# Kernel optimization log

Measured on AMD Instinct MI355X. Metric: run time of the kernel, lower is better.

The kernel has to match this reference:

```python
import jax, jax.numpy as jnp
import numpy as np

IN_DIM = 1024
OUT_DIM = 1024
SPLINE_ORDER = 3
NUM_KNOTS = 16
BATCH = 2048


def _bspline_bases(t, knots, order):
    # t: (N,) flattened inputs; knots: (NUM_KNOTS,)
    # degree-0 indicator bases, then Cox-de Boor recursion (matches torch slicing)
    tb = t[:, None]  # (N, 1) broadcasts against knot slices
    b = ((knots[:-1] <= tb) & (knots[1:] > tb)).astype(t.dtype)  # (N, NUM_KNOTS-1)
    for k in range(1, order):
        left = (tb - knots[:-k - 1]) / (knots[k:-1] - knots[:-k - 1]) * b[:, :-1]
        right = (knots[k + 1:] - tb) / (knots[k + 1:] - knots[1:-k]) * b[:, 1:]
        b = left + right
    return b  # (N, NUM_KNOTS - order)


def setup_inputs() -> dict:
    key = jax.random.key(0)
    k1, k2 = jax.random.split(key)
    x = jax.random.uniform(k1, (BATCH, IN_DIM), dtype=jnp.float32)
    spline_parameters = jax.random.normal(
        k2, (OUT_DIM, IN_DIM, NUM_KNOTS - SPLINE_ORDER), dtype=jnp.float32
    )
    w_b = jnp.array(1.0, dtype=jnp.float32)
    w_s = jnp.array(1.0, dtype=jnp.float32)
    return {"x": x, "spline_parameters": spline_parameters, "w_b": w_b, "w_s": w_s}


def reference(x, spline_parameters, w_b, w_s):
    knots = jnp.linspace(-1.0 - 2.0 / NUM_KNOTS, 1.0 + 2.0 / NUM_KNOTS, NUM_KNOTS,
                         dtype=x.dtype)
    bases = _bspline_bases(x.reshape(-1), knots, SPLINE_ORDER)  # (B*I, K)
    bases = bases.reshape(*x.shape, -1)  # (B, I, K)
    # sum over in_dim and knots directly (avoids the (B, O, I, K) intermediate);
    # equals sum_i of (w_b*silu(x)[b,i] + w_s*splines[b,o,i]) from the torch code.
    splines = jnp.einsum("bik,oik->bo", bases, spline_parameters)  # (B, O)
    silu_sum = jnp.sum(jax.nn.silu(x), axis=-1, keepdims=True)  # (B, 1)
    return w_b * silu_sum + w_s * splines
```

## Files before the change

### kernel.cpp

```cpp
#include <hip/hip_runtime.h>
#include <hip/hip_bf16.h>
#include <cstdint>
#include <cstddef>

#define IN_DIM 1024
#define OUT_DIM 1024
#define BATCH 2048
#define NSEG 8
#define K2 (IN_DIM * NSEG)

typedef float f32x4 __attribute__((ext_vector_type(4)));
typedef __bf16 bf16x8 __attribute__((ext_vector_type(8)));

__device__ __forceinline__ unsigned int f2bf(float f) {
  unsigned int u = __float_as_uint(f);
  u += 0x7FFF + ((u >> 16) & 1);
  return u >> 16;
}

__device__ __forceinline__ void gload16(const void* g, void* l) {
  __builtin_amdgcn_global_load_lds((__attribute__((address_space(1))) void*)g,
                                   (__attribute__((address_space(3))) void*)l,
                                   16, 0, 0);
}

__device__ __forceinline__ uint4 basis8(float v) {
  float u = (v + 1.125f) * (1.0f / 0.15f);
  int j = (int)floorf(u);
  j = j < 7 ? 7 : (j > 14 ? 14 : j);
  float s = u - (float)j;
  unsigned long long w0 = f2bf(0.5f * (1.f - s) * (1.f - s));
  unsigned long long w1 = f2bf(0.5f + s * (1.f - s));
  unsigned long long w2 = f2bf(0.5f * s * s);
  unsigned __int128 pack = (unsigned __int128)(w0 | (w1 << 16) | (w2 << 32))
                           << (16 * (j - 7));
  unsigned long long lo = (unsigned long long)pack;
  unsigned long long hi = (unsigned long long)(pack >> 64);
  uint4 o;
  o.x = (unsigned int)lo; o.y = (unsigned int)(lo >> 32);
  o.z = (unsigned int)hi; o.w = (unsigned int)(hi >> 32);
  return o;
}

__global__ __launch_bounds__(256) void silu_init(const float* __restrict__ x,
                                                 float* __restrict__ out,
                                                 const float* __restrict__ wbp) {
  __shared__ float red[4];
  const int b = blockIdx.x;
  const int t = threadIdx.x;
  float4 xv = ((const float4*)(x + (size_t)b * IN_DIM))[t];
  float lsum = xv.x / (1.f + __expf(-xv.x)) + xv.y / (1.f + __expf(-xv.y)) +
               xv.z / (1.f + __expf(-xv.z)) + xv.w / (1.f + __expf(-xv.w));
#pragma unroll
  for (int off = 32; off >= 1; off >>= 1) lsum += __shfl_down(lsum, off);
  if ((t & 63) == 0) red[t >> 6] = lsum;
  __syncthreads();
  float v = wbp[0] * (red[0] + red[1] + red[2] + red[3]);
  float4 vv = {v, v, v, v};
  ((float4*)(out + (size_t)b * OUT_DIM))[t] = vv;
}

__global__ __launch_bounds__(256) void prep_b(const float* __restrict__ p,
                                              short* __restrict__ B,
                                              const float* __restrict__ wsp) {
  __shared__ float ld[3328];
  const int blk = blockIdx.x;
  const int t = threadIdx.x;
  const uint4* src = (const uint4*)(p + (size_t)blk * 3328);
  uint4* l4 = (uint4*)ld;
#pragma unroll
  for (int c = 0; c < 3; ++c) l4[c * 256 + t] = src[c * 256 + t];
  if (t < 64) l4[768 + t] = src[768 + t];
  __syncthreads();
  const float* my = ld + t * 13 + 5;
  const float w = wsp[0];
  uint4 o;
  o.x = f2bf(w * my[0]) | (f2bf(w * my[1]) << 16);
  o.y = f2bf(w * my[2]) | (f2bf(w * my[3]) << 16);
  o.z = f2bf(w * my[4]) | (f2bf(w * my[5]) << 16);
  o.w = f2bf(w * my[6]) | (f2bf(w * my[7]) << 16);
  ((uint4*)B)[(size_t)blk * 256 + t] = o;
}

#define BM 64
#define BN 256
#define BK 32
#define KSPLIT 4
#define KPB (K2 / KSPLIT)
#define KSTEPS (KPB / BK)

__global__ __launch_bounds__(256) void gemm_fused(const float* __restrict__ x,
                                                  const short* __restrict__ B,
                                                  float* __restrict__ out) {
  __shared__ __bf16 As[2][BM][BK];
  __shared__ __bf16 Bs[2][BN][BK];

  const int tid = threadIdx.x;
  const int wid = tid >> 6;
  const int lane = tid & 63;
  const int bm = blockIdx.x >> 2;
  const int bn = blockIdx.x & 3;
  const int ks = blockIdx.y;
  const int row0 = bm * BM;
  const int col0 = bn * BN;
  const int kstart = ks * KPB;
  const int istart = kstart / NSEG;

  const int sr = lane >> 2;
  const int sc = (lane & 3) * 8;
  const short* bg = B + (size_t)(col0 + 64 * wid + sr) * K2 + kstart + sc;

  const float* xp = x + (size_t)(row0 + (tid >> 2)) * IN_DIM + istart + (tid & 3);

  f32x4 acc[4][4];
#pragma unroll
  for (int m = 0; m < 4; ++m)
#pragma unroll
    for (int n = 0; n < 4; ++n) acc[m][n] = (f32x4){0.f, 0.f, 0.f, 0.f};

  const int wc = 64 * wid;
  const int fr = lane & 15;
  const int fk = (lane >> 4) * 8;

#define STAGE_B(kt_, buf_)                                                    \
  {                                                                           \
    const int kb_ = (kt_)*BK;                                                 \
    _Pragma("unroll") for (int c = 0; c < 4; ++c)                             \
        gload16(bg + (size_t)(c * 16) * K2 + kb_,                             \
                &Bs[buf_][64 * wid + c * 16][0]);                             \
  }

#define COMPUTE(buf_)                                                         \
  {                                                                           \
    bf16x8 af[4], bb[4];                                                      \
    _Pragma("unroll") for (int m = 0; m < 4; ++m)                             \
        af[m] = *(const bf16x8*)&As[buf_][m * 16 + fr][fk];                   \
    _Pragma("unroll") for (int n = 0; n < 4; ++n)                             \
        bb[n] = *(const bf16x8*)&Bs[buf_][wc + n * 16 + fr][fk];              \
    _Pragma("unroll") for (int m = 0; m < 4; ++m)                             \
        _Pragma("unroll") for (int n = 0; n < 4; ++n)                         \
            acc[m][n] = __builtin_amdgcn_mfma_f32_16x16x32_bf16(              \
                af[m], bb[n], acc[m][n], 0, 0, 0);                            \
  }

#define LDS_BARRIER                                                           \
  asm volatile("s_waitcnt lgkmcnt(0)" ::: "memory");                          \
  __builtin_amdgcn_s_barrier();

  float xa = xp[0];
  float xb = xp[4];
  STAGE_B(0, 0);
  ((uint4*)As[0])[tid] = basis8(xa);
  LDS_BARRIER;

#pragma unroll 1
  for (int i = 0; i < (KSTEPS - 2) / 2; ++i) {
    const int t0 = 2 * i;
    STAGE_B(t0 + 1, 1);
    ((uint4*)As[1])[tid] = basis8(xb);
    xa = xp[(t0 + 2) * 4];
    asm volatile("s_waitcnt vmcnt(5)" ::: "memory");
    COMPUTE(0);
    LDS_BARRIER;
    STAGE_B(t0 + 2, 0);
    ((uint4*)As[0])[tid] = basis8(xa);
    xb = xp[(t0 + 3) * 4];
    asm volatile("s_waitcnt vmcnt(5)" ::: "memory");
    COMPUTE(1);
    LDS_BARRIER;
  }

  STAGE_B(KSTEPS - 1, 1);
  ((uint4*)As[1])[tid] = basis8(xb);
  asm volatile("s_waitcnt vmcnt(4)" ::: "memory");
  COMPUTE(0);
  LDS_BARRIER;

  asm volatile("s_waitcnt vmcnt(0)" ::: "memory");
  COMPUTE(1);

#undef STAGE_B
#undef COMPUTE
#undef LDS_BARRIER

  const int orow = (lane >> 4) * 4;
#pragma unroll
  for (int m = 0; m < 4; ++m)
#pragma unroll
    for (int n = 0; n < 4; ++n) {
      const int rg = row0 + m * 16 + orow;
      const int cg = col0 + wc + n * 16 + fr;
      float* op = out + (size_t)rg * OUT_DIM + cg;
#pragma unroll
      for (int r = 0; r < 4; ++r)
        atomicAdd(op + (size_t)r * OUT_DIM, acc[m][n][r]);
    }
}

extern "C" void kernel_launch(void* const* d_in, const int* in_sizes, int n_in,
                              void* d_out, int out_size, void* d_ws, size_t ws_size,
                              hipStream_t stream) {
  const float* x = (const float*)d_in[0];
  const float* p = (const float*)d_in[1];
  const float* wb = (const float*)d_in[2];
  const float* wsc = (const float*)d_in[3];
  float* out = (float*)d_out;

  short* B = (short*)d_ws;

  silu_init<<<BATCH, 256, 0, stream>>>(x, out, wb);
  prep_b<<<OUT_DIM * IN_DIM / 256, 256, 0, stream>>>(p, B, wsc);
  dim3 grid(128, KSPLIT);
  gemm_fused<<<grid, 256, 0, stream>>>(x, B, out);
}
```

Baseline: 172.3 us.

## Merge prep kernels, enlarge GEMM tile to 128x256 with triple-buffered B

Merges the SiLU init and weight-conversion kernels into one launch, which removes one kernel launch. The GEMM tile grows to BM=128 with 512 threads (8 waves in a 2x4 layout) and the K-split rises to 8. B staging moves to a triple-buffered pipeline with deeper prefetch of x values, and the block index is remapped so K-split blocks are grouped. The basis computation uses packed bf16 conversion and select-based placement in place of a 128-bit shift. This adds more atomic traffic from the higher K-split and more register pressure.

```diff
diff --git a/kernel.cpp b/kernel.cpp
--- a/kernel.cpp
+++ b/kernel.cpp
@@ -9,11 +9,18 @@
 #define NSEG 8
 #define K2 (IN_DIM * NSEG)
 
+#define BM 128
+#define BN 256
+#define BK 32
+#define KSPLIT 8
+#define KPB (K2 / KSPLIT)
+#define KSTEPS (KPB / BK)
+
 typedef float f32x4 __attribute__((ext_vector_type(4)));
 typedef __bf16 bf16x8 __attribute__((ext_vector_type(8)));
 
-__device__ __forceinline__ unsigned int f2bf(float f) {
-  unsigned int u = __float_as_uint(f);
+__device__ __forceinline__ unsigned f2bf(float f) {
+  unsigned u = __float_as_uint(f);
   u += 0x7FFF + ((u >> 16) & 1);
   return u >> 16;
 }
@@ -25,90 +32,88 @@
 }
 
 __device__ __forceinline__ uint4 basis8(float v) {
-  float u = (v + 1.125f) * (1.0f / 0.15f);
-  int j = (int)floorf(u);
-  j = j < 7 ? 7 : (j > 14 ? 14 : j);
-  float s = u - (float)j;
-  unsigned long long w0 = f2bf(0.5f * (1.f - s) * (1.f - s));
-  unsigned long long w1 = f2bf(0.5f + s * (1.f - s));
-  unsigned long long w2 = f2bf(0.5f * s * s);
-  unsigned __int128 pack = (unsigned __int128)(w0 | (w1 << 16) | (w2 << 32))
-                           << (16 * (j - 7));
-  unsigned long long lo = (unsigned long long)pack;
-  unsigned long long hi = (unsigned long long)(pack >> 64);
+  float u = __builtin_fmaf(v, 1.0f / 0.15f, 7.5f);
+  float jf = floorf(u);
+  int j = (int)jf;
+  float s = u - jf;
+  float t1 = 1.f - s;
+  float w0 = 0.5f * t1 * t1;
+  float w1 = __builtin_fmaf(s, t1, 0.5f);
+  float w2 = 0.5f * s * s;
+  unsigned d0, d1;
+  asm("v_cvt_pk_bf16_f32 %0, %1, %2" : "=v"(d0) : "v"(w0), "v"(w1));
+  asm("v_cvt_pk_bf16_f32 %0, %1, %2" : "=v"(d1) : "v"(w2), "v"(0.f));
+  int p = j - 7;
+  unsigned long long full = (((unsigned long long)d1 << 32) | d0) << ((p & 1) << 4);
+  unsigned lo = (unsigned)full, hi = (unsigned)(full >> 32);
+  int q = p >> 1;
   uint4 o;
-  o.x = (unsigned int)lo; o.y = (unsigned int)(lo >> 32);
-  o.z = (unsigned int)hi; o.w = (unsigned int)(hi >> 32);
+  o.x = q == 0 ? lo : 0u;
+  o.y = q == 1 ? lo : (q == 0 ? hi : 0u);
+  o.z = q == 2 ? lo : (q == 1 ? hi : 0u);
+  o.w = q == 3 ? lo : (q == 2 ? hi : 0u);
   return o;
 }
 
-__global__ __launch_bounds__(256) void silu_init(const float* __restrict__ x,
-                                                 float* __restrict__ out,
-                                                 const float* __restrict__ wbp) {
-  __shared__ float red[4];
-  const int b = blockIdx.x;
-  const int t = threadIdx.x;
-  float4 xv = ((const float4*)(x + (size_t)b * IN_DIM))[t];
-  float lsum = xv.x / (1.f + __expf(-xv.x)) + xv.y / (1.f + __expf(-xv.y)) +
-               xv.z / (1.f + __expf(-xv.z)) + xv.w / (1.f + __expf(-xv.w));
-#pragma unroll
-  for (int off = 32; off >= 1; off >>= 1) lsum += __shfl_down(lsum, off);
-  if ((t & 63) == 0) red[t >> 6] = lsum;
-  __syncthreads();
-  float v = wbp[0] * (red[0] + red[1] + red[2] + red[3]);
-  float4 vv = {v, v, v, v};
-  ((float4*)(out + (size_t)b * OUT_DIM))[t] = vv;
-}
-
-__global__ __launch_bounds__(256) void prep_b(const float* __restrict__ p,
-                                              short* __restrict__ B,
-                                              const float* __restrict__ wsp) {
+__global__ __launch_bounds__(256) void prep(const float* __restrict__ p,
+                                            const float* __restrict__ x,
+                                            short* __restrict__ B,
+                                            float* __restrict__ out,
+                                            const float* __restrict__ wbp,
+                                            const float* __restrict__ wsp) {
   __shared__ float ld[3328];
   const int blk = blockIdx.x;
   const int t = threadIdx.x;
-  const uint4* src = (const uint4*)(p + (size_t)blk * 3328);
-  uint4* l4 = (uint4*)ld;
-#pragma unroll
-  for (int c = 0; c < 3; ++c) l4[c * 256 + t] = src[c * 256 + t];
-  if (t < 64) l4[768 + t] = src[768 + t];
-  __syncthreads();
-  const float* my = ld + t * 13 + 5;
-  const float w = wsp[0];
-  uint4 o;
-  o.x = f2bf(w * my[0]) | (f2bf(w * my[1]) << 16);
-  o.y = f2bf(w * my[2]) | (f2bf(w * my[3]) << 16);
-  o.z = f2bf(w * my[4]) | (f2bf(w * my[5]) << 16);
-  o.w = f2bf(w * my[6]) | (f2bf(w * my[7]) << 16);
-  ((uint4*)B)[(size_t)blk * 256 + t] = o;
-}
-
-#define BM 64
-#define BN 256
-#define BK 32
-#define KSPLIT 4
-#define KPB (K2 / KSPLIT)
-#define KSTEPS (KPB / BK)
-
-__global__ __launch_bounds__(256) void gemm_fused(const float* __restrict__ x,
+  if (blk < 4096) {
+    const uint4* src = (const uint4*)(p + (size_t)blk * 3328);
+    uint4* l4 = (uint4*)ld;
+#pragma unroll
+    for (int c = 0; c < 3; ++c) l4[c * 256 + t] = src[c * 256 + t];
+    if (t < 64) l4[768 + t] = src[768 + t];
+    __syncthreads();
+    const float* my = ld + t * 13 + 5;
+    const float w = wsp[0];
+    uint4 o;
+    o.x = f2bf(w * my[0]) | (f2bf(w * my[1]) << 16);
+    o.y = f2bf(w * my[2]) | (f2bf(w * my[3]) << 16);
+    o.z = f2bf(w * my[4]) | (f2bf(w * my[5]) << 16);
+    o.w = f2bf(w * my[6]) | (f2bf(w * my[7]) << 16);
+    ((uint4*)B)[(size_t)blk * 256 + t] = o;
+  } else {
+    const int b = blk - 4096;
+    float4 xv = ((const float4*)(x + (size_t)b * IN_DIM))[t];
+    float lsum = xv.x / (1.f + __expf(-xv.x)) + xv.y / (1.f + __expf(-xv.y)) +
+                 xv.z / (1.f + __expf(-xv.z)) + xv.w / (1.f + __expf(-xv.w));
+#pragma unroll
+    for (int off = 32; off >= 1; off >>= 1) lsum += __shfl_down(lsum, off);
+    if ((t & 63) == 0) ld[t >> 6] = lsum;
+    __syncthreads();
+    float v = wbp[0] * (ld[0] + ld[1] + ld[2] + ld[3]);
+    float4 vv = {v, v, v, v};
+    ((float4*)(out + (size_t)b * OUT_DIM))[t] = vv;
+  }
+}
+
+__global__ __launch_bounds__(512) void gemm_fused(const float* __restrict__ x,
                                                   const short* __restrict__ B,
                                                   float* __restrict__ out) {
   __shared__ __bf16 As[2][BM][BK];
-  __shared__ __bf16 Bs[2][BN][BK];
+  __shared__ __bf16 Bs[3][BN][BK];
 
   const int tid = threadIdx.x;
   const int wid = tid >> 6;
   const int lane = tid & 63;
-  const int bm = blockIdx.x >> 2;
-  const int bn = blockIdx.x & 3;
-  const int ks = blockIdx.y;
+  const int bid = blockIdx.x;
+  const int ks = bid & 7;
+  const int bm = (bid >> 3) & 15;
+  const int bn = bid >> 7;
   const int row0 = bm * BM;
   const int col0 = bn * BN;
   const int kstart = ks * KPB;
   const int istart = kstart / NSEG;
 
-  const int sr = lane >> 2;
-  const int sc = (lane & 3) * 8;
-  const short* bg = B + (size_t)(col0 + 64 * wid + sr) * K2 + kstart + sc;
+  const short* bg = B + (size_t)(col0 + 32 * wid + (lane >> 2)) * K2 + kstart +
+                    (lane & 3) * 8;
 
   const float* xp = x + (size_t)(row0 + (tid >> 2)) * IN_DIM + istart + (tid & 3);
 
@@ -118,67 +123,69 @@
 #pragma unroll
     for (int n = 0; n < 4; ++n) acc[m][n] = (f32x4){0.f, 0.f, 0.f, 0.f};
 
-  const int wc = 64 * wid;
+  const int wr = (wid >> 2) * 64;
+  const int wc = (wid & 3) * 64;
   const int fr = lane & 15;
   const int fk = (lane >> 4) * 8;
 
 #define STAGE_B(kt_, buf_)                                                    \
   {                                                                           \
     const int kb_ = (kt_)*BK;                                                 \
-    _Pragma("unroll") for (int c = 0; c < 4; ++c)                             \
-        gload16(bg + (size_t)(c * 16) * K2 + kb_,                             \
-                &Bs[buf_][64 * wid + c * 16][0]);                             \
-  }
-
-#define COMPUTE(buf_)                                                         \
+    gload16(bg + kb_, &Bs[buf_][32 * wid][0]);                                \
+    gload16(bg + (size_t)16 * K2 + kb_, &Bs[buf_][32 * wid + 16][0]);         \
+  }
+
+#define COMPUTE(A_, B_)                                                       \
   {                                                                           \
-    bf16x8 af[4], bb[4];                                                      \
-    _Pragma("unroll") for (int m = 0; m < 4; ++m)                             \
-        af[m] = *(const bf16x8*)&As[buf_][m * 16 + fr][fk];                   \
-    _Pragma("unroll") for (int n = 0; n < 4; ++n)                             \
-        bb[n] = *(const bf16x8*)&Bs[buf_][wc + n * 16 + fr][fk];              \
-    _Pragma("unroll") for (int m = 0; m < 4; ++m)                             \
-        _Pragma("unroll") for (int n = 0; n < 4; ++n)                         \
-            acc[m][n] = __builtin_amdgcn_mfma_f32_16x16x32_bf16(              \
-                af[m], bb[n], acc[m][n], 0, 0, 0);                            \
+    bf16x8 af_[4], bb_[4];                                                    \
+    _Pragma("unroll") for (int m_ = 0; m_ < 4; ++m_)                          \
+        af_[m_] = *(const bf16x8*)&(A_)[wr + m_ * 16 + fr][fk];               \
+    _Pragma("unroll") for (int n_ = 0; n_ < 4; ++n_)                          \
+        bb_[n_] = *(const bf16x8*)&(B_)[wc + n_ * 16 + fr][fk];               \
+    _Pragma("unroll") for (int m_ = 0; m_ < 4; ++m_)                          \
+        _Pragma("unroll") for (int n_ = 0; n_ < 4; ++n_)                      \
+            acc[m_][n_] = __builtin_amdgcn_mfma_f32_16x16x32_bf16(            \
+                af_[m_], bb_[n_], acc[m_][n_], 0, 0, 0);                      \
   }
 
 #define LDS_BARRIER                                                           \
   asm volatile("s_waitcnt lgkmcnt(0)" ::: "memory");                          \
   __builtin_amdgcn_s_barrier();
 
-  float xa = xp[0];
-  float xb = xp[4];
+  float xc = xp[0];
   STAGE_B(0, 0);
-  ((uint4*)As[0])[tid] = basis8(xa);
+  STAGE_B(1, 1);
+  float xn0 = xp[4];
+  float xn1 = xp[8];
+  ((uint4*)As[0])[tid] = basis8(xc);
+  asm volatile("s_waitcnt vmcnt(0)" ::: "memory");
   LDS_BARRIER;
 
+  float xnew;
+#define STEP(s_)                                                              \
+  {                                                                           \
+    const int t_ = 6 * i + (s_);                                              \
+    STAGE_B(t_ + 2, ((s_) + 2) % 3);                                          \
+    ((uint4*)As[((s_) + 1) & 1])[tid] = basis8(xn0);                          \
+    { int tn_ = t_ + 3; tn_ = tn_ > 31 ? 31 : tn_; xnew = xp[tn_ * 4]; }      \
+    COMPUTE(As[(s_) & 1], Bs[(s_) % 3]);                                      \
+    asm volatile("s_waitcnt vmcnt(3)" ::: "memory");                          \
+    LDS_BARRIER;                                                              \
+    xn0 = xn1; xn1 = xnew;                                                    \
+  }
+
 #pragma unroll 1
-  for (int i = 0; i < (KSTEPS - 2) / 2; ++i) {
-    const int t0 = 2 * i;
-    STAGE_B(t0 + 1, 1);
-    ((uint4*)As[1])[tid] = basis8(xb);
-    xa = xp[(t0 + 2) * 4];
-    asm volatile("s_waitcnt vmcnt(5)" ::: "memory");
-    COMPUTE(0);
-    LDS_BARRIER;
-    STAGE_B(t0 + 2, 0);
-    ((uint4*)As[0])[tid] = basis8(xa);
-    xb = xp[(t0 + 3) * 4];
-    asm volatile("s_waitcnt vmcnt(5)" ::: "memory");
-    COMPUTE(1);
-    LDS_BARRIER;
-  }
-
-  STAGE_B(KSTEPS - 1, 1);
-  ((uint4*)As[1])[tid] = basis8(xb);
-  asm volatile("s_waitcnt vmcnt(4)" ::: "memory");
-  COMPUTE(0);
+  for (int i = 0; i < 5; ++i) {
+    STEP(0) STEP(1) STEP(2) STEP(3) STEP(4) STEP(5)
+  }
+
+  ((uint4*)As[1])[tid] = basis8(xn0);
+  COMPUTE(As[0], Bs[0]);
+  asm volatile("s_waitcnt vmcnt(0)" ::: "memory");
   LDS_BARRIER;
-
-  asm volatile("s_waitcnt vmcnt(0)" ::: "memory");
-  COMPUTE(1);
-
+  COMPUTE(As[1], Bs[1]);
+
+#undef STEP
 #undef STAGE_B
 #undef COMPUTE
 #undef LDS_BARRIER
@@ -188,7 +195,7 @@
   for (int m = 0; m < 4; ++m)
 #pragma unroll
     for (int n = 0; n < 4; ++n) {
-      const int rg = row0 + m * 16 + orow;
+      const int rg = row0 + wr + m * 16 + orow;
       const int cg = col0 + wc + n * 16 + fr;
       float* op = out + (size_t)rg * OUT_DIM + cg;
 #pragma unroll
@@ -208,8 +215,6 @@
 
   short* B = (short*)d_ws;
 
-  silu_init<<<BATCH, 256, 0, stream>>>(x, out, wb);
-  prep_b<<<OUT_DIM * IN_DIM / 256, 256, 0, stream>>>(p, B, wsc);
-  dim3 grid(128, KSPLIT);
-  gemm_fused<<<grid, 256, 0, stream>>>(x, B, out);
-}
+  prep<<<6144, 256, 0, stream>>>(p, x, B, out, wb, wsc);
+  gemm_fused<<<512, 512, 0, stream>>>(x, B, out);
+}
```

New measurement: 208.9 us. 1.21x slower.

## Merge prep kernels, double K-split, reorder block mapping, cheapen basis packing

Applied to the files above, without the earlier changes.

Merges the silu row-sum initialisation and the spline-weight bf16 conversion into one launch, with branches selected by block index. Doubles the K-split of the fused GEMM from 4 to 8 (1024 blocks) and remaps block IDs so consecutive blocks share the same output tile across K slices. The basis computation now uses packed bf16 conversion instructions and select-based placement instead of 128-bit shifts. It also adds sched_barrier fences after LDS barriers. The extra K-split doubles the atomicAdd traffic on the output in exchange for more parallelism.

```diff
diff --git a/kernel.cpp b/kernel.cpp
--- a/kernel.cpp
+++ b/kernel.cpp
@@ -9,11 +9,18 @@
 #define NSEG 8
 #define K2 (IN_DIM * NSEG)
 
+#define BM 64
+#define BN 256
+#define BK 32
+#define KSPLIT 8
+#define KPB (K2 / KSPLIT)
+#define KSTEPS (KPB / BK)
+
 typedef float f32x4 __attribute__((ext_vector_type(4)));
 typedef __bf16 bf16x8 __attribute__((ext_vector_type(8)));
 
-__device__ __forceinline__ unsigned int f2bf(float f) {
-  unsigned int u = __float_as_uint(f);
+__device__ __forceinline__ unsigned f2bf(float f) {
+  unsigned u = __float_as_uint(f);
   u += 0x7FFF + ((u >> 16) & 1);
   return u >> 16;
 }
@@ -25,69 +32,67 @@
 }
 
 __device__ __forceinline__ uint4 basis8(float v) {
-  float u = (v + 1.125f) * (1.0f / 0.15f);
-  int j = (int)floorf(u);
-  j = j < 7 ? 7 : (j > 14 ? 14 : j);
-  float s = u - (float)j;
-  unsigned long long w0 = f2bf(0.5f * (1.f - s) * (1.f - s));
-  unsigned long long w1 = f2bf(0.5f + s * (1.f - s));
-  unsigned long long w2 = f2bf(0.5f * s * s);
-  unsigned __int128 pack = (unsigned __int128)(w0 | (w1 << 16) | (w2 << 32))
-                           << (16 * (j - 7));
-  unsigned long long lo = (unsigned long long)pack;
-  unsigned long long hi = (unsigned long long)(pack >> 64);
+  float u = __builtin_fmaf(v, 1.0f / 0.15f, 7.5f);
+  float jf = floorf(u);
+  int j = (int)jf;
+  float s = u - jf;
+  float t1 = 1.f - s;
+  float w0 = 0.5f * t1 * t1;
+  float w1 = __builtin_fmaf(s, t1, 0.5f);
+  float w2 = 0.5f * s * s;
+  unsigned d0, d1;
+  asm("v_cvt_pk_bf16_f32 %0, %1, %2" : "=v"(d0) : "v"(w0), "v"(w1));
+  asm("v_cvt_pk_bf16_f32 %0, %1, %2" : "=v"(d1) : "v"(w2), "v"(0.f));
+  int p = j - 7;
+  unsigned long long full = (((unsigned long long)d1 << 32) | d0) << ((p & 1) << 4);
+  unsigned lo = (unsigned)full, hi = (unsigned)(full >> 32);
+  int q = p >> 1;
   uint4 o;
-  o.x = (unsigned int)lo; o.y = (unsigned int)(lo >> 32);
-  o.z = (unsigned int)hi; o.w = (unsigned int)(hi >> 32);
+  o.x = q == 0 ? lo : 0u;
+  o.y = q == 1 ? lo : (q == 0 ? hi : 0u);
+  o.z = q == 2 ? lo : (q == 1 ? hi : 0u);
+  o.w = q == 3 ? lo : (q == 2 ? hi : 0u);
   return o;
 }
 
-__global__ __launch_bounds__(256) void silu_init(const float* __restrict__ x,
-                                                 float* __restrict__ out,
-                                                 const float* __restrict__ wbp) {
-  __shared__ float red[4];
-  const int b = blockIdx.x;
-  const int t = threadIdx.x;
-  float4 xv = ((const float4*)(x + (size_t)b * IN_DIM))[t];
-  float lsum = xv.x / (1.f + __expf(-xv.x)) + xv.y / (1.f + __expf(-xv.y)) +
-               xv.z / (1.f + __expf(-xv.z)) + xv.w / (1.f + __expf(-xv.w));
-#pragma unroll
-  for (int off = 32; off >= 1; off >>= 1) lsum += __shfl_down(lsum, off);
-  if ((t & 63) == 0) red[t >> 6] = lsum;
-  __syncthreads();
-  float v = wbp[0] * (red[0] + red[1] + red[2] + red[3]);
-  float4 vv = {v, v, v, v};
-  ((float4*)(out + (size_t)b * OUT_DIM))[t] = vv;
-}
-
-__global__ __launch_bounds__(256) void prep_b(const float* __restrict__ p,
-                                              short* __restrict__ B,
-                                              const float* __restrict__ wsp) {
+__global__ __launch_bounds__(256) void prep(const float* __restrict__ p,
+                                            const float* __restrict__ x,
+                                            short* __restrict__ B,
+                                            float* __restrict__ out,
+                                            const float* __restrict__ wbp,
+                                            const float* __restrict__ wsp) {
   __shared__ float ld[3328];
   const int blk = blockIdx.x;
   const int t = threadIdx.x;
-  const uint4* src = (const uint4*)(p + (size_t)blk * 3328);
-  uint4* l4 = (uint4*)ld;
-#pragma unroll
-  for (int c = 0; c < 3; ++c) l4[c * 256 + t] = src[c * 256 + t];
-  if (t < 64) l4[768 + t] = src[768 + t];
-  __syncthreads();
-  const float* my = ld + t * 13 + 5;
-  const float w = wsp[0];
-  uint4 o;
-  o.x = f2bf(w * my[0]) | (f2bf(w * my[1]) << 16);
-  o.y = f2bf(w * my[2]) | (f2bf(w * my[3]) << 16);
-  o.z = f2bf(w * my[4]) | (f2bf(w * my[5]) << 16);
-  o.w = f2bf(w * my[6]) | (f2bf(w * my[7]) << 16);
-  ((uint4*)B)[(size_t)blk * 256 + t] = o;
-}
-
-#define BM 64
-#define BN 256
-#define BK 32
-#define KSPLIT 4
-#define KPB (K2 / KSPLIT)
-#define KSTEPS (KPB / BK)
+  if (blk < 4096) {
+    const uint4* src = (const uint4*)(p + (size_t)blk * 3328);
+    uint4* l4 = (uint4*)ld;
+#pragma unroll
+    for (int c = 0; c < 3; ++c) l4[c * 256 + t] = src[c * 256 + t];
+    if (t < 64) l4[768 + t] = src[768 + t];
+    __syncthreads();
+    const float* my = ld + t * 13 + 5;
+    const float w = wsp[0];
+    uint4 o;
+    o.x = f2bf(w * my[0]) | (f2bf(w * my[1]) << 16);
+    o.y = f2bf(w * my[2]) | (f2bf(w * my[3]) << 16);
+    o.z = f2bf(w * my[4]) | (f2bf(w * my[5]) << 16);
+    o.w = f2bf(w * my[6]) | (f2bf(w * my[7]) << 16);
+    ((uint4*)B)[(size_t)blk * 256 + t] = o;
+  } else {
+    const int b = blk - 4096;
+    float4 xv = ((const float4*)(x + (size_t)b * IN_DIM))[t];
+    float lsum = xv.x / (1.f + __expf(-xv.x)) + xv.y / (1.f + __expf(-xv.y)) +
+                 xv.z / (1.f + __expf(-xv.z)) + xv.w / (1.f + __expf(-xv.w));
+#pragma unroll
+    for (int off = 32; off >= 1; off >>= 1) lsum += __shfl_down(lsum, off);
+    if ((t & 63) == 0) ld[t >> 6] = lsum;
+    __syncthreads();
+    float v = wbp[0] * (ld[0] + ld[1] + ld[2] + ld[3]);
+    float4 vv = {v, v, v, v};
+    ((float4*)(out + (size_t)b * OUT_DIM))[t] = vv;
+  }
+}
 
 __global__ __launch_bounds__(256) void gemm_fused(const float* __restrict__ x,
                                                   const short* __restrict__ B,
@@ -98,9 +103,10 @@
   const int tid = threadIdx.x;
   const int wid = tid >> 6;
   const int lane = tid & 63;
-  const int bm = blockIdx.x >> 2;
-  const int bn = blockIdx.x & 3;
-  const int ks = blockIdx.y;
+  const int bid = blockIdx.x;
+  const int ks = bid & 7;
+  const int bm = (bid >> 3) & 31;
+  const int bn = bid >> 8;
   const int row0 = bm * BM;
   const int col0 = bn * BN;
   const int kstart = ks * KPB;
@@ -145,7 +151,9 @@
 
 #define LDS_BARRIER                                                           \
   asm volatile("s_waitcnt lgkmcnt(0)" ::: "memory");                          \
-  __builtin_amdgcn_s_barrier();
+  __builtin_amdgcn_s_barrier();                                               \
+  asm volatile("" ::: "memory");                                              \
+  __builtin_amdgcn_sched_barrier(0);
 
   float xa = xp[0];
   float xb = xp[4];
@@ -208,8 +216,6 @@
 
   short* B = (short*)d_ws;
 
-  silu_init<<<BATCH, 256, 0, stream>>>(x, out, wb);
-  prep_b<<<OUT_DIM * IN_DIM / 256, 256, 0, stream>>>(p, B, wsc);
-  dim3 grid(128, KSPLIT);
-  gemm_fused<<<grid, 256, 0, stream>>>(x, B, out);
-}
+  prep<<<6144, 256, 0, stream>>>(p, x, B, out, wb, wsc);
+  gemm_fused<<<1024, 256, 0, stream>>>(x, B, out);
+}
```

Measured after the change: 184.3 us. 7.0% more time.
